# Optimization experiments

Hardware: AMD Instinct MI355X
Metric: run time of the kernel (lower is better)

Reference implementation:

```python
import jax, jax.numpy as jnp
import numpy as np

N, D, C, G, NNZ = 256, 1024, 50000, 4, 300000
EPS = 1e-5


def setup_inputs() -> dict:
    key = jax.random.key(0)
    ks = jax.random.split(key, 5)
    return {
        "output": jax.random.normal(ks[0], (N, D), jnp.float32),
        "wt2_w": jax.random.normal(ks[1], (C, D), jnp.float32) * 0.02,
        "wt2_b": jnp.zeros((C,), jnp.float32),
        "A_vals": jax.random.uniform(ks[2], (G, NNZ), dtype=jnp.float32),
        "vec": jnp.ones((G,), jnp.float32),
        "A_rows": jax.random.randint(ks[3], (G, NNZ), 0, C, jnp.int32),
        "A_cols": jax.random.randint(ks[4], (G, NNZ), 0, C, jnp.int32),
    }


def reference(output, wt2_w, wt2_b, A_vals, vec, A_rows, A_cols):
    # BatchNorm1d(embed_dim, affine=False), training-mode batch stats (biased var)
    mean = jnp.mean(output, axis=0)
    var = jnp.var(output, axis=0)
    h0 = (output - mean) * jax.lax.rsqrt(var + EPS)
    # wt2 linear + swish -> Z [N, C]
    h1 = h0 @ wt2_w.T + wt2_b
    Z = h1 * jax.nn.sigmoid(h1)
    # multi-graph sparse propagation: neighbors += spmm(A_i * vec[i], Z^T)^T
    # spmm out[b, r] = sum_{e: rows[e]==r} vals[e] * Z[b, cols[e]]
    Zt = Z.T  # [C, N]
    neighbors = jnp.zeros_like(Z)
    n_graphs = A_vals.shape[0]
    for i in range(n_graphs):  # small fixed number of relation graphs
        vals = A_vals[i] * vec[i]               # learnable per-graph weight
        msgs = Zt[A_cols[i]] * vals[:, None]    # [nnz, N] gathered messages
        agg = jax.ops.segment_sum(msgs, A_rows[i], num_segments=Zt.shape[0])  # [C, N]
        neighbors = neighbors + agg.T
    # residual combine
    return neighbors + Z
```

## Files before the change

kernel.cpp:

```cpp
#include <hip/hip_runtime.h>

typedef __attribute__((ext_vector_type(8))) short short8;
typedef __attribute__((ext_vector_type(4))) float floatx4;

#define C_DIM 50000
#define D_DIM 1024
#define N_DIM 256
#define G_NUM 4
#define NNZ_G 300000
#define E_TOT (G_NUM * NNZ_G)

#define O_SB   0u
#define O_H0   8192u
#define O_ZT   532480u
#define O_CNT  26132480u
#define O_OFF  26332544u
#define O_CUR  26532608u
#define O_BS   26732672u
#define O_EDG  26733696u

static __device__ __forceinline__ unsigned short f2bf(float f) {
    union { float f; unsigned u; } v; v.f = f;
    unsigned r = v.u + 0x7fffu + ((v.u >> 16) & 1u);
    return (unsigned short)(r >> 16);
}
static __device__ __forceinline__ float bf2f(unsigned short u) {
    union { unsigned u; float f; } v; v.u = ((unsigned)u) << 16;
    return v.f;
}

__global__ __launch_bounds__(256) void k_bnstats(const float* __restrict__ x,
                                                 float* __restrict__ scale,
                                                 float* __restrict__ bias) {
    __shared__ float sms[8][32], smss[8][32];
    const int t = threadIdx.x;
    const int dc = t & 31, grp = t >> 5;
    const int d = blockIdx.x * 32 + dc;
    float s = 0.f, ss = 0.f;
    for (int n = grp; n < N_DIM; n += 8) {
        float v = x[n * D_DIM + d];
        s += v; ss += v * v;
    }
    sms[grp][dc] = s; smss[grp][dc] = ss;
    __syncthreads();
    if (t < 32) {
        float S = 0.f, SS = 0.f;
#pragma unroll
        for (int g2 = 0; g2 < 8; ++g2) { S += sms[g2][t]; SS += smss[g2][t]; }
        float mean = S * (1.f / N_DIM);
        float var  = SS * (1.f / N_DIM) - mean * mean;
        float sc = rsqrtf(var + 1e-5f);
        int dd = blockIdx.x * 32 + t;
        scale[dd] = sc;
        bias[dd] = -mean * sc;
    }
}

__global__ __launch_bounds__(256) void k_h0f(const float* __restrict__ x,
                                             const float* __restrict__ scale,
                                             const float* __restrict__ bias,
                                             unsigned short* __restrict__ h0F) {
    int id = blockIdx.x * 256 + threadIdx.x;
    int b = id >> 7, kc = id & 127;
    const float4* xp = (const float4*)&x[(size_t)b * D_DIM + kc * 8];
    float4 f0 = xp[0], f1 = xp[1];
    const float4* sp = (const float4*)&scale[kc * 8];
    const float4* bp = (const float4*)&bias[kc * 8];
    float4 s0 = sp[0], s1 = sp[1], b0 = bp[0], b1 = bp[1];
    short8 o;
    o[0] = (short)f2bf(f0.x * s0.x + b0.x);
    o[1] = (short)f2bf(f0.y * s0.y + b0.y);
    o[2] = (short)f2bf(f0.z * s0.z + b0.z);
    o[3] = (short)f2bf(f0.w * s0.w + b0.w);
    o[4] = (short)f2bf(f1.x * s1.x + b1.x);
    o[5] = (short)f2bf(f1.y * s1.y + b1.y);
    o[6] = (short)f2bf(f1.z * s1.z + b1.z);
    o[7] = (short)f2bf(f1.w * s1.w + b1.w);
    int off = (b >> 4) * 16384 + (kc >> 2) * 512 + (kc & 3) * 128 + (b & 15) * 8;
    *(short8*)&h0F[off] = o;
}

__global__ __launch_bounds__(256) void k_gemm(const float* __restrict__ W,
                                              const float* __restrict__ wb,
                                              const unsigned short* __restrict__ h0F,
                                              unsigned short* __restrict__ Zt) {
    __shared__ unsigned short A_lds[2][8 * 64 * 8];
    const int t = threadIdx.x;
    const int w = t >> 6, lane = t & 63;
    const int m = lane & 15, g = lane >> 4;
    const int c0 = blockIdx.x * 64;

    const int srow = t >> 4;
    const int scc  = t & 15;
    const int s_kh = scc >> 3;
    const int s_g  = (scc >> 1) & 3;
    const int s_half = scc & 1;
    const int sbase = (srow + 16 * s_g) * 8 + s_half * 4;

    const unsigned short* hb = h0F + (size_t)(w * 4) * 16384 + lane * 8;

    float4 raA[4], raB[4];
    floatx4 acc[4][4];
#pragma unroll
    for (int i = 0; i < 4; ++i)
#pragma unroll
        for (int j = 0; j < 4; ++j) acc[i][j] = (floatx4)0.f;

#define LOADA(RA, ksv)                                                           \
    {                                                                            \
        const int kkv = (ksv) * 64;                                              \
        _Pragma("unroll")                                                        \
        for (int q = 0; q < 4; ++q) {                                            \
            int rr_ = c0 + q * 16 + srow; if (rr_ >= C_DIM) rr_ = C_DIM - 1;     \
            RA[q] = *(const float4*)&W[(size_t)rr_ * D_DIM + kkv + scc * 4];     \
        }                                                                        \
    }
#define STOREA(RA, bufv)                                                          \
    {                                                                             \
        _Pragma("unroll")                                                         \
        for (int q = 0; q < 4; ++q) {                                             \
            float4 f_ = RA[q];                                                    \
            unsigned p0_ = (unsigned)f2bf(f_.x) | ((unsigned)f2bf(f_.y) << 16);   \
            unsigned p1_ = (unsigned)f2bf(f_.z) | ((unsigned)f2bf(f_.w) << 16);   \
            *(uint2*)&A_lds[bufv][(s_kh * 4 + q) * 512 + sbase] =                 \
                make_uint2(p0_, p1_);                                             \
        }                                                                         \
    }
#define BARRIER()                                               \
    asm volatile("s_waitcnt lgkmcnt(0)" ::: "memory");          \
    __builtin_amdgcn_sched_barrier(0);                          \
    __builtin_amdgcn_s_barrier();                               \
    __builtin_amdgcn_sched_barrier(0);

#define GSTEP(ksv, RAs, RAl, CUR)                                                 \
    {                                                                             \
        short8 bfrag[2][4];                                                       \
        _Pragma("unroll")                                                         \
        for (int kh = 0; kh < 2; ++kh)                                            \
            _Pragma("unroll")                                                     \
            for (int j = 0; j < 4; ++j)                                           \
                bfrag[kh][j] = *(const short8*)&hb[(size_t)j * 16384 +            \
                                                  ((ksv) * 2 + kh) * 512];        \
        short8 afrag[2][4];                                                       \
        _Pragma("unroll")                                                         \
        for (int kh = 0; kh < 2; ++kh)                                            \
            _Pragma("unroll")                                                     \
            for (int i = 0; i < 4; ++i)                                           \
                afrag[kh][i] = *(const short8*)&A_lds[CUR][(kh * 4 + i) * 512 +   \
                                                          lane * 8];              \
        if ((ksv) < 15) STOREA(RAs, (CUR) ^ 1)                                    \
        if ((ksv) < 14) LOADA(RAl, (ksv) + 2)                                     \
        __builtin_amdgcn_s_setprio(1);                                            \
        _Pragma("unroll")                                                         \
        for (int kh = 0; kh < 2; ++kh)                                            \
            _Pragma("unroll")                                                     \
            for (int i = 0; i < 4; ++i)                                           \
                _Pragma("unroll")                                                 \
                for (int j = 0; j < 4; ++j)                                       \
                    acc[i][j] = __builtin_amdgcn_mfma_f32_16x16x32_bf16(          \
                        afrag[kh][i], bfrag[kh][j], acc[i][j], 0, 0, 0);          \
        __builtin_amdgcn_s_setprio(0);                                            \
        BARRIER()                                                                 \
    }

    LOADA(raA, 0)
    STOREA(raA, 0)
    LOADA(raB, 1)
    BARRIER()

#pragma unroll 1
    for (int ks2 = 0; ks2 < 16; ks2 += 2) {
        GSTEP(ks2,     raB, raA, 0)
        GSTEP(ks2 + 1, raA, raB, 1)
    }
#undef GSTEP
#undef LOADA
#undef STOREA
#undef BARRIER

#pragma unroll
    for (int i = 0; i < 4; ++i) {
#pragma unroll
        for (int j = 0; j < 4; ++j) {
            int b = w * 64 + j * 16 + m;
#pragma unroll
            for (int rr = 0; rr < 4; ++rr) {
                int c = c0 + i * 16 + g * 4 + rr;
                if (c < C_DIM) {
                    float x = acc[i][j][rr] + wb[c];
                    float z = x / (1.f + __expf(-x));
                    Zt[(size_t)c * 256 + b] = f2bf(z);
                }
            }
        }
    }
}

__global__ __launch_bounds__(256) void k_count(const int* __restrict__ rows,
                                               int* __restrict__ counts) {
    int id = blockIdx.x * 256 + threadIdx.x;
    if (id < E_TOT) atomicAdd(&counts[rows[id]], 1);
}

__global__ __launch_bounds__(256) void k_scan1(const int* __restrict__ counts,
                                               int* __restrict__ offsets,
                                               int* __restrict__ bsums) {
    __shared__ int sm[256];
    int t = threadIdx.x, i = blockIdx.x * 256 + t;
    int v = (i < C_DIM) ? counts[i] : 0;
    sm[t] = v; __syncthreads();
    for (int off = 1; off < 256; off <<= 1) {
        int x = (t >= off) ? sm[t - off] : 0;
        __syncthreads();
        sm[t] += x;
        __syncthreads();
    }
    if (i < C_DIM) offsets[i] = sm[t] - v;
    if (t == 255) bsums[blockIdx.x] = sm[255];
}

__global__ __launch_bounds__(256) void k_scan2(int* __restrict__ bsums,
                                               int* __restrict__ offsets) {
    __shared__ int sm[256];
    int t = threadIdx.x;
    int v = (t < 196) ? bsums[t] : 0;
    sm[t] = v; __syncthreads();
    for (int off = 1; off < 256; off <<= 1) {
        int x = (t >= off) ? sm[t - off] : 0;
        __syncthreads();
        sm[t] += x;
        __syncthreads();
    }
    if (t < 196) bsums[t] = sm[t] - v;
    if (t == 0) offsets[C_DIM] = sm[255];
}

__global__ __launch_bounds__(256) void k_scan3(const int* __restrict__ bsums,
                                               int* __restrict__ offsets,
                                               int* __restrict__ cursor) {
    int i = blockIdx.x * 256 + threadIdx.x;
    if (i < C_DIM) {
        int off = offsets[i] + bsums[blockIdx.x];
        offsets[i] = off;
        cursor[i] = off;
    }
}

__global__ __launch_bounds__(256) void k_scatter(const int* __restrict__ rows,
                                                 const int* __restrict__ cols,
                                                 const float* __restrict__ vals,
                                                 const float* __restrict__ vec,
                                                 int* __restrict__ cursor,
                                                 int2* __restrict__ edges) {
    int id = blockIdx.x * 256 + threadIdx.x;
    if (id < E_TOT) {
        int gidx = id / NNZ_G;
        float v = vals[id] * vec[gidx];
        int r = rows[id];
        int c = cols[id];
        int pos = atomicAdd(&cursor[r], 1);
        edges[pos] = make_int2(c, __float_as_int(v));
    }
}

__global__ __launch_bounds__(256) void k_agg(const unsigned short* __restrict__ Zt,
                                             const int* __restrict__ offsets,
                                             const int2* __restrict__ edges,
                                             float* __restrict__ out) {
    __shared__ float sm[32 * 256];
    const int t = threadIdx.x;
    const int w = t >> 6, lane = t & 63;
    const int r0 = blockIdx.x * 32;
    const int h = lane & 31;
    const int eh = lane >> 5;
    const int base = h * 8;

#pragma unroll 1
    for (int k = 0; k < 8; ++k) {
        int lrow = w * 8 + k;
        int r = __builtin_amdgcn_readfirstlane(r0 + lrow);
        if (r < C_DIM) {
            float a[8];
            {
                short8 z = *(const short8*)&Zt[(size_t)r * 256 + base];
                float zm = eh ? 0.f : 1.f;
#pragma unroll
                for (int j = 0; j < 8; ++j) a[j] = zm * bf2f((unsigned short)z[j]);
            }
            int s = offsets[r], e = offsets[r + 1];
            for (; s + 4 <= e; s += 4) {
                int2 ea = edges[s + eh];
                int2 eb = edges[s + 2 + eh];
                short8 ga = *(const short8*)&Zt[(size_t)(unsigned)ea.x * 256 + base];
                short8 gb = *(const short8*)&Zt[(size_t)(unsigned)eb.x * 256 + base];
                float va = __int_as_float(ea.y), vb = __int_as_float(eb.y);
#pragma unroll
                for (int j = 0; j < 8; ++j)
                    a[j] += va * bf2f((unsigned short)ga[j]) + vb * bf2f((unsigned short)gb[j]);
            }
            for (; s + 2 <= e; s += 2) {
                int2 ea = edges[s + eh];
                short8 ga = *(const short8*)&Zt[(size_t)(unsigned)ea.x * 256 + base];
                float va = __int_as_float(ea.y);
#pragma unroll
                for (int j = 0; j < 8; ++j)
                    a[j] += va * bf2f((unsigned short)ga[j]);
            }
            if (s < e) {
                int2 e0 = edges[s];
                short8 g0 = *(const short8*)&Zt[(size_t)(unsigned)e0.x * 256 + base];
                float v0 = eh ? 0.f : __int_as_float(e0.y);
#pragma unroll
                for (int j = 0; j < 8; ++j)
                    a[j] += v0 * bf2f((unsigned short)g0[j]);
            }
#pragma unroll
            for (int j = 0; j < 8; ++j) a[j] += __shfl_xor(a[j], 32);
            if (eh == 0) {
                *(float4*)&sm[lrow * 256 + base]     = make_float4(a[0], a[1], a[2], a[3]);
                *(float4*)&sm[lrow * 256 + base + 4] = make_float4(a[4], a[5], a[6], a[7]);
            }
        }
    }
    __syncthreads();

    int rows = C_DIM - r0; if (rows > 32) rows = 32;
    int nq = rows >> 2;
    float4* op = (float4*)&out[(size_t)t * C_DIM + r0];
#pragma unroll 1
    for (int q = 0; q < nq; ++q) {
        float4 o;
        o.x = sm[(q * 4 + 0) * 256 + t];
        o.y = sm[(q * 4 + 1) * 256 + t];
        o.z = sm[(q * 4 + 2) * 256 + t];
        o.w = sm[(q * 4 + 3) * 256 + t];
        op[q] = o;
    }
}

extern "C" void kernel_launch(void* const* d_in, const int* in_sizes, int n_in,
                              void* d_out, int out_size, void* d_ws, size_t ws_size,
                              hipStream_t stream) {
    (void)in_sizes; (void)n_in; (void)out_size; (void)ws_size;
    const float* x     = (const float*)d_in[0];
    const float* W     = (const float*)d_in[1];
    const float* wb    = (const float*)d_in[2];
    const float* Avals = (const float*)d_in[3];
    const float* vec   = (const float*)d_in[4];
    const int*   Arows = (const int*)d_in[5];
    const int*   Acols = (const int*)d_in[6];
    float* out = (float*)d_out;
    char* ws = (char*)d_ws;

    float* scale = (float*)(ws + O_SB);
    float* bias  = scale + 1024;
    unsigned short* h0F = (unsigned short*)(ws + O_H0);
    unsigned short* Zt  = (unsigned short*)(ws + O_ZT);
    int* counts  = (int*)(ws + O_CNT);
    int* offsets = (int*)(ws + O_OFF);
    int* cursor  = (int*)(ws + O_CUR);
    int* bsums   = (int*)(ws + O_BS);
    int2* edges  = (int2*)(ws + O_EDG);

    hipMemsetAsync(counts, 0, C_DIM * sizeof(int), stream);

    k_bnstats<<<32, 256, 0, stream>>>(x, scale, bias);
    k_h0f<<<128, 256, 0, stream>>>(x, scale, bias, h0F);
    k_count<<<(E_TOT + 255) / 256, 256, 0, stream>>>(Arows, counts);
    k_gemm<<<(C_DIM + 63) / 64, 256, 0, stream>>>(W, wb, h0F, Zt);
    k_scan1<<<196, 256, 0, stream>>>(counts, offsets, bsums);
    k_scan2<<<1, 256, 0, stream>>>(bsums, offsets);
    k_scan3<<<196, 256, 0, stream>>>(bsums, offsets, cursor);
    k_scatter<<<(E_TOT + 255) / 256, 256, 0, stream>>>(Arows, Acols, Avals, vec, cursor, edges);
    k_agg<<<(C_DIM + 31) / 32, 256, 0, stream>>>(Zt, offsets, edges, out);
}
```

Measured before the change: 625.1 us.

## Load GEMM weight fragments directly to registers, dropping LDS staging and barriers

The wt2 GEMM kernel no longer stages W tiles in shared memory with double buffering and barriers. Each wave now loads its A fragments straight from global memory into registers, converts them to bf16 in place, and owns a 32x128 output tile instead of 64x64. Loads for the next k-step are issued before the MFMAs of the current one. This removes LDS traffic and block syncs, but each W row is now fetched by two waves and the global A loads are less coalesced, with more register pressure from eight B fragments per step.

```diff
diff --git a/kernel.cpp b/kernel.cpp
--- a/kernel.cpp
+++ b/kernel.cpp
@@ -27,6 +27,15 @@
 static __device__ __forceinline__ float bf2f(unsigned short u) {
     union { unsigned u; float f; } v; v.u = ((unsigned)u) << 16;
     return v.f;
+}
+
+static __device__ __forceinline__ short8 cvt8(float4 a, float4 b) {
+    short8 r;
+    r[0] = (short)f2bf(a.x); r[1] = (short)f2bf(a.y);
+    r[2] = (short)f2bf(a.z); r[3] = (short)f2bf(a.w);
+    r[4] = (short)f2bf(b.x); r[5] = (short)f2bf(b.y);
+    r[6] = (short)f2bf(b.z); r[7] = (short)f2bf(b.w);
+    return r;
 }
 
 __global__ __launch_bounds__(256) void k_bnstats(const float* __restrict__ x,
@@ -84,108 +93,70 @@
                                               const float* __restrict__ wb,
                                               const unsigned short* __restrict__ h0F,
                                               unsigned short* __restrict__ Zt) {
-    __shared__ unsigned short A_lds[2][8 * 64 * 8];
     const int t = threadIdx.x;
     const int w = t >> 6, lane = t & 63;
     const int m = lane & 15, g = lane >> 4;
-    const int c0 = blockIdx.x * 64;
-
-    const int srow = t >> 4;
-    const int scc  = t & 15;
-    const int s_kh = scc >> 3;
-    const int s_g  = (scc >> 1) & 3;
-    const int s_half = scc & 1;
-    const int sbase = (srow + 16 * s_g) * 8 + s_half * 4;
-
-    const unsigned short* hb = h0F + (size_t)(w * 4) * 16384 + lane * 8;
-
-    float4 raA[4], raB[4];
-    floatx4 acc[4][4];
-#pragma unroll
-    for (int i = 0; i < 4; ++i)
-#pragma unroll
-        for (int j = 0; j < 4; ++j) acc[i][j] = (floatx4)0.f;
-
-#define LOADA(RA, ksv)                                                           \
-    {                                                                            \
-        const int kkv = (ksv) * 64;                                              \
-        _Pragma("unroll")                                                        \
-        for (int q = 0; q < 4; ++q) {                                            \
-            int rr_ = c0 + q * 16 + srow; if (rr_ >= C_DIM) rr_ = C_DIM - 1;     \
-            RA[q] = *(const float4*)&W[(size_t)rr_ * D_DIM + kkv + scc * 4];     \
-        }                                                                        \
-    }
-#define STOREA(RA, bufv)                                                          \
-    {                                                                             \
-        _Pragma("unroll")                                                         \
-        for (int q = 0; q < 4; ++q) {                                             \
-            float4 f_ = RA[q];                                                    \
-            unsigned p0_ = (unsigned)f2bf(f_.x) | ((unsigned)f2bf(f_.y) << 16);   \
-            unsigned p1_ = (unsigned)f2bf(f_.z) | ((unsigned)f2bf(f_.w) << 16);   \
-            *(uint2*)&A_lds[bufv][(s_kh * 4 + q) * 512 + sbase] =                 \
-                make_uint2(p0_, p1_);                                             \
-        }                                                                         \
-    }
-#define BARRIER()                                               \
-    asm volatile("s_waitcnt lgkmcnt(0)" ::: "memory");          \
-    __builtin_amdgcn_sched_barrier(0);                          \
-    __builtin_amdgcn_s_barrier();                               \
-    __builtin_amdgcn_sched_barrier(0);
-
-#define GSTEP(ksv, RAs, RAl, CUR)                                                 \
-    {                                                                             \
-        short8 bfrag[2][4];                                                       \
-        _Pragma("unroll")                                                         \
-        for (int kh = 0; kh < 2; ++kh)                                            \
-            _Pragma("unroll")                                                     \
-            for (int j = 0; j < 4; ++j)                                           \
-                bfrag[kh][j] = *(const short8*)&hb[(size_t)j * 16384 +            \
-                                                  ((ksv) * 2 + kh) * 512];        \
-        short8 afrag[2][4];                                                       \
-        _Pragma("unroll")                                                         \
-        for (int kh = 0; kh < 2; ++kh)                                            \
-            _Pragma("unroll")                                                     \
-            for (int i = 0; i < 4; ++i)                                           \
-                afrag[kh][i] = *(const short8*)&A_lds[CUR][(kh * 4 + i) * 512 +   \
-                                                          lane * 8];              \
-        if ((ksv) < 15) STOREA(RAs, (CUR) ^ 1)                                    \
-        if ((ksv) < 14) LOADA(RAl, (ksv) + 2)                                     \
-        __builtin_amdgcn_s_setprio(1);                                            \
-        _Pragma("unroll")                                                         \
-        for (int kh = 0; kh < 2; ++kh)                                            \
-            _Pragma("unroll")                                                     \
-            for (int i = 0; i < 4; ++i)                                           \
-                _Pragma("unroll")                                                 \
-                for (int j = 0; j < 4; ++j)                                       \
-                    acc[i][j] = __builtin_amdgcn_mfma_f32_16x16x32_bf16(          \
-                        afrag[kh][i], bfrag[kh][j], acc[i][j], 0, 0, 0);          \
-        __builtin_amdgcn_s_setprio(0);                                            \
-        BARRIER()                                                                 \
-    }
-
-    LOADA(raA, 0)
-    STOREA(raA, 0)
-    LOADA(raB, 1)
-    BARRIER()
-
+    const int cb = blockIdx.x * 64 + (w & 1) * 32;
+    const int nh = w >> 1;
+
+    int ra0 = cb + m;      if (ra0 >= C_DIM) ra0 = C_DIM - 1;
+    int ra1 = cb + 16 + m; if (ra1 >= C_DIM) ra1 = C_DIM - 1;
+    const float* pA0 = &W[(size_t)ra0 * D_DIM + g * 8];
+    const float* pA1 = &W[(size_t)ra1 * D_DIM + g * 8];
+    const unsigned short* hb = h0F + (size_t)(nh * 8) * 16384 + lane * 8;
+
+    floatx4 acc[2][8];
+#pragma unroll
+    for (int i = 0; i < 2; ++i)
+#pragma unroll
+        for (int j = 0; j < 8; ++j) acc[i][j] = (floatx4)0.f;
+
+#define LOADN(A0L, A0H, A1L, A1H, NB, ksv)                                    \
+    {                                                                         \
+        const int kkv = (ksv) * 32;                                           \
+        A0L = *(const float4*)(pA0 + kkv);                                    \
+        A0H = *(const float4*)(pA0 + kkv + 4);                                \
+        A1L = *(const float4*)(pA1 + kkv);                                    \
+        A1H = *(const float4*)(pA1 + kkv + 4);                                \
+        _Pragma("unroll")                                                     \
+        for (int j = 0; j < 8; ++j)                                           \
+            NB[j] = *(const short8*)&hb[(size_t)j * 16384 + (ksv) * 512];     \
+    }
+
+#define STEP(A0L, A0H, A1L, A1H, CB, nA0L, nA0H, nA1L, nA1H, NB, ksv)         \
+    {                                                                         \
+        if ((ksv) < 31) LOADN(nA0L, nA0H, nA1L, nA1H, NB, (ksv) + 1)          \
+        short8 af0 = cvt8(A0L, A0H);                                          \
+        short8 af1 = cvt8(A1L, A1H);                                          \
+        _Pragma("unroll")                                                     \
+        for (int j = 0; j < 8; ++j) {                                         \
+            acc[0][j] = __builtin_amdgcn_mfma_f32_16x16x32_bf16(              \
+                af0, CB[j], acc[0][j], 0, 0, 0);                              \
+            acc[1][j] = __builtin_amdgcn_mfma_f32_16x16x32_bf16(              \
+                af1, CB[j], acc[1][j], 0, 0, 0);                              \
+        }                                                                     \
+    }
+
+    float4 xa0, xa1, xa2, xa3, ya0, ya1, ya2, ya3;
+    short8 xb[8], yb[8];
+
+    LOADN(xa0, xa1, xa2, xa3, xb, 0)
 #pragma unroll 1
-    for (int ks2 = 0; ks2 < 16; ks2 += 2) {
-        GSTEP(ks2,     raB, raA, 0)
-        GSTEP(ks2 + 1, raA, raB, 1)
-    }
-#undef GSTEP
-#undef LOADA
-#undef STOREA
-#undef BARRIER
-
-#pragma unroll
-    for (int i = 0; i < 4; ++i) {
-#pragma unroll
-        for (int j = 0; j < 4; ++j) {
-            int b = w * 64 + j * 16 + m;
+    for (int ks2 = 0; ks2 < 32; ks2 += 2) {
+        STEP(xa0, xa1, xa2, xa3, xb, ya0, ya1, ya2, ya3, yb, ks2)
+        STEP(ya0, ya1, ya2, ya3, yb, xa0, xa1, xa2, xa3, xb, ks2 + 1)
+    }
+#undef STEP
+#undef LOADN
+
+#pragma unroll
+    for (int i = 0; i < 2; ++i) {
+#pragma unroll
+        for (int j = 0; j < 8; ++j) {
+            int b = nh * 128 + j * 16 + m;
 #pragma unroll
             for (int rr = 0; rr < 4; ++rr) {
-                int c = c0 + i * 16 + g * 4 + rr;
+                int c = cb + i * 16 + g * 4 + rr;
                 if (c < C_DIM) {
                     float x = acc[i][j][rr] + wb[c];
                     float z = x / (1.f + __expf(-x));
```

New measurement: 665.7 us. +6.5%, slower.

## Chunk Z^T by 32-batch columns and split aggregation over a batch-chunk grid

Applied to the files above, without the earlier changes.

The GEMM epilogue now writes Z^T in 8 chunks of 32 batch columns ([8][C][32] bf16), so one gathered row slice is 64 contiguous bytes. The aggregation kernel uses a 2D grid (row blocks × batch chunks). Each wavefront handles 4 edges at a time, 16 lanes per edge and 2 bf16 per lane, and combines partial sums with shuffles. The aim is to shrink the gathered Z^T working set per block and improve cache locality, at the cost of reading each edge list 8 times and issuing smaller gathers.

```diff
diff --git a/kernel.cpp b/kernel.cpp
--- a/kernel.cpp
+++ b/kernel.cpp
@@ -183,13 +183,14 @@
 #pragma unroll
         for (int j = 0; j < 4; ++j) {
             int b = w * 64 + j * 16 + m;
+            unsigned short* zt = Zt + (size_t)(b >> 5) * (C_DIM * 32) + (b & 31);
 #pragma unroll
             for (int rr = 0; rr < 4; ++rr) {
                 int c = c0 + i * 16 + g * 4 + rr;
                 if (c < C_DIM) {
                     float x = acc[i][j][rr] + wb[c];
                     float z = x / (1.f + __expf(-x));
-                    Zt[(size_t)c * 256 + b] = f2bf(z);
+                    zt[(size_t)c * 32] = f2bf(z);
                 }
             }
         }
@@ -263,78 +264,65 @@
     }
 }
 
-__global__ __launch_bounds__(256) void k_agg(const unsigned short* __restrict__ Zt,
+__global__ __launch_bounds__(256) void k_agg(const unsigned short* __restrict__ ZtC,
                                              const int* __restrict__ offsets,
                                              const int2* __restrict__ edges,
                                              float* __restrict__ out) {
-    __shared__ float sm[32 * 256];
+    __shared__ float sm[128 * 32];
     const int t = threadIdx.x;
     const int w = t >> 6, lane = t & 63;
-    const int r0 = blockIdx.x * 32;
-    const int h = lane & 31;
-    const int eh = lane >> 5;
-    const int base = h * 8;
+    const int eg = lane >> 4, bp = lane & 15;
+    const int r0 = blockIdx.x * 128;
+    const int b0 = blockIdx.y * 32;
+    const unsigned short* zc = ZtC + (size_t)blockIdx.y * (C_DIM * 32);
 
 #pragma unroll 1
-    for (int k = 0; k < 8; ++k) {
-        int lrow = w * 8 + k;
+    for (int k = 0; k < 32; ++k) {
+        int lrow = w * 32 + k;
         int r = __builtin_amdgcn_readfirstlane(r0 + lrow);
         if (r < C_DIM) {
-            float a[8];
-            {
-                short8 z = *(const short8*)&Zt[(size_t)r * 256 + base];
-                float zm = eh ? 0.f : 1.f;
-#pragma unroll
-                for (int j = 0; j < 8; ++j) a[j] = zm * bf2f((unsigned short)z[j]);
+            float a0 = 0.f, a1 = 0.f, d0 = 0.f, d1 = 0.f;
+            int s = offsets[r], e = offsets[r + 1];
+#pragma unroll 1
+            for (; s < e; s += 8) {
+                int i1 = s + eg, i2 = s + 4 + eg;
+                int2 e1 = edges[i1 < e ? i1 : e - 1];
+                int2 e2 = edges[i2 < e ? i2 : e - 1];
+                float v1 = (i1 < e) ? __int_as_float(e1.y) : 0.f;
+                float v2 = (i2 < e) ? __int_as_float(e2.y) : 0.f;
+                unsigned g1 = *(const unsigned*)&zc[(size_t)(unsigned)e1.x * 32 + bp * 2];
+                unsigned g2 = *(const unsigned*)&zc[(size_t)(unsigned)e2.x * 32 + bp * 2];
+                a0 += v1 * bf2f((unsigned short)g1);
+                a1 += v1 * bf2f((unsigned short)(g1 >> 16));
+                d0 += v2 * bf2f((unsigned short)g2);
+                d1 += v2 * bf2f((unsigned short)(g2 >> 16));
             }
-            int s = offsets[r], e = offsets[r + 1];
-            for (; s + 4 <= e; s += 4) {
-                int2 ea = edges[s + eh];
-                int2 eb = edges[s + 2 + eh];
-                short8 ga = *(const short8*)&Zt[(size_t)(unsigned)ea.x * 256 + base];
-                short8 gb = *(const short8*)&Zt[(size_t)(unsigned)eb.x * 256 + base];
-                float va = __int_as_float(ea.y), vb = __int_as_float(eb.y);
-#pragma unroll
-                for (int j = 0; j < 8; ++j)
-                    a[j] += va * bf2f((unsigned short)ga[j]) + vb * bf2f((unsigned short)gb[j]);
-            }
-            for (; s + 2 <= e; s += 2) {
-                int2 ea = edges[s + eh];
-                short8 ga = *(const short8*)&Zt[(size_t)(unsigned)ea.x * 256 + base];
-                float va = __int_as_float(ea.y);
-#pragma unroll
-                for (int j = 0; j < 8; ++j)
-                    a[j] += va * bf2f((unsigned short)ga[j]);
-            }
-            if (s < e) {
-                int2 e0 = edges[s];
-                short8 g0 = *(const short8*)&Zt[(size_t)(unsigned)e0.x * 256 + base];
-                float v0 = eh ? 0.f : __int_as_float(e0.y);
-#pragma unroll
-                for (int j = 0; j < 8; ++j)
-                    a[j] += v0 * bf2f((unsigned short)g0[j]);
-            }
-#pragma unroll
-            for (int j = 0; j < 8; ++j) a[j] += __shfl_xor(a[j], 32);
-            if (eh == 0) {
-                *(float4*)&sm[lrow * 256 + base]     = make_float4(a[0], a[1], a[2], a[3]);
-                *(float4*)&sm[lrow * 256 + base + 4] = make_float4(a[4], a[5], a[6], a[7]);
+            a0 += d0; a1 += d1;
+            a0 += __shfl_xor(a0, 16); a0 += __shfl_xor(a0, 32);
+            a1 += __shfl_xor(a1, 16); a1 += __shfl_xor(a1, 32);
+            if (eg == 0) {
+                unsigned rz = *(const unsigned*)&zc[(size_t)r * 32 + bp * 2];
+                a0 += bf2f((unsigned short)rz);
+                a1 += bf2f((unsigned short)(rz >> 16));
+                *(float2*)&sm[lrow * 32 + bp * 2] = make_float2(a0, a1);
             }
         }
     }
     __syncthreads();
 
-    int rows = C_DIM - r0; if (rows > 32) rows = 32;
-    int nq = rows >> 2;
-    float4* op = (float4*)&out[(size_t)t * C_DIM + r0];
-#pragma unroll 1
-    for (int q = 0; q < nq; ++q) {
-        float4 o;
-        o.x = sm[(q * 4 + 0) * 256 + t];
-        o.y = sm[(q * 4 + 1) * 256 + t];
-        o.z = sm[(q * 4 + 2) * 256 + t];
-        o.w = sm[(q * 4 + 3) * 256 + t];
-        op[q] = o;
+    const int b = t & 31, seg = t >> 5;
+    float* op = &out[(size_t)(b0 + b) * C_DIM + r0 + seg * 16];
+#pragma unroll
+    for (int q = 0; q < 4; ++q) {
+        int rb = seg * 16 + q * 4;
+        if (r0 + rb < C_DIM) {
+            float4 o;
+            o.x = sm[(rb + 0) * 32 + b];
+            o.y = sm[(rb + 1) * 32 + b];
+            o.z = sm[(rb + 2) * 32 + b];
+            o.w = sm[(rb + 3) * 32 + b];
+            *(float4*)&op[q * 4] = o;
+        }
     }
 }
 
@@ -355,7 +343,7 @@
     float* scale = (float*)(ws + O_SB);
     float* bias  = scale + 1024;
     unsigned short* h0F = (unsigned short*)(ws + O_H0);
-    unsigned short* Zt  = (unsigned short*)(ws + O_ZT);
+    unsigned short* ZtC = (unsigned short*)(ws + O_ZT);
     int* counts  = (int*)(ws + O_CNT);
     int* offsets = (int*)(ws + O_OFF);
     int* cursor  = (int*)(ws + O_CUR);
@@ -367,10 +355,10 @@
     k_bnstats<<<32, 256, 0, stream>>>(x, scale, bias);
     k_h0f<<<128, 256, 0, stream>>>(x, scale, bias, h0F);
     k_count<<<(E_TOT + 255) / 256, 256, 0, stream>>>(Arows, counts);
-    k_gemm<<<(C_DIM + 63) / 64, 256, 0, stream>>>(W, wb, h0F, Zt);
+    k_gemm<<<(C_DIM + 63) / 64, 256, 0, stream>>>(W, wb, h0F, ZtC);
     k_scan1<<<196, 256, 0, stream>>>(counts, offsets, bsums);
     k_scan2<<<1, 256, 0, stream>>>(bsums, offsets);
     k_scan3<<<196, 256, 0, stream>>>(bsums, offsets, cursor);
     k_scatter<<<(E_TOT + 255) / 256, 256, 0, stream>>>(Arows, Acols, Avals, vec, cursor, edges);
-    k_agg<<<(C_DIM + 31) / 32, 256, 0, stream>>>(Zt, offsets, edges, out);
-}
+    k_agg<<<dim3(391, 8), 256, 0, stream>>>(ZtC, offsets, edges, out);
+}
```

After: 720.4 us. +15.2%, slower.
